# Optimization experiments

Hardware: AMD Instinct MI355X
Metric: run time of the kernel (lower is better)

Reference implementation:

```python
import jax, jax.numpy as jnp
import numpy as np
from jax import lax

CHANNEL_N = 16
ALPHA_CHANNEL = 3
FIRE_RATE = 0.5


def get_sobel(size):
    # generalized Sobel: g(x,y) = x / (x^2 + y^2), zero at center
    s = size // 2
    yy, xx = np.mgrid[-s:s + 1, -s:s + 1].astype(np.float32)
    denom = xx * xx + yy * yy
    denom[s, s] = 1.0
    gx = xx / denom
    gy = yy / denom
    gx /= np.sum(np.abs(gx))
    gy /= np.sum(np.abs(gy))
    return gx, gy


def build_kernel(C):
    # stack the six sobel stencils (sizes 3/5/7), zero-padded to 7x7 so a single
    # SAME depthwise conv reproduces the three separate padded convs exactly
    ks = []
    for size in (3, 5, 7):
        gx, gy = get_sobel(size)
        p = (7 - size) // 2
        ks.append(np.pad(gx, p))
        ks.append(np.pad(gy, p))
    k = np.stack(ks, 0)                # [6,7,7]
    k = np.tile(k, (C, 1, 1))          # [6C,7,7], channel-major groups
    return jnp.asarray(k.transpose(1, 2, 0)[:, :, None, :])  # HWIO [7,7,1,6C]


def _maxpool(x, size):
    p = size // 2
    return lax.reduce_window(x, -jnp.inf, lax.max, (1, size, size, 1), (1, 1, 1, 1),
                             [(0, 0), (p, p), (p, p), (0, 0)])


def _life_mask(x):
    alpha = x[..., ALPHA_CHANNEL:ALPHA_CHANNEL + 1]
    return _maxpool(alpha, 3) > 0.1


def _update(x, stoch_u, valid_mask, kern, W0, b0, W1):
    N, H, W, C = x.shape
    pre_life = _life_mask(x)
    y = lax.conv_general_dilated(x, kern, (1, 1), [(3, 3), (3, 3)],
                                 dimension_numbers=("NHWC", "HWIO", "NHWC"),
                                 feature_group_count=C)  # [N,H,W,6C] channel-major
    # reorder to (y1 all C, y2 all C, ...) matching torch.cat order
    y = y.reshape(N, H, W, C, 6).transpose(0, 1, 2, 4, 3).reshape(N, H, W, 6 * C)
    perc = jnp.concatenate([x, y, _maxpool(x, 5)], axis=-1)  # [N,H,W,8C]
    h = jax.nn.relu(perc @ W0 + b0)  # [N,H,W,256]
    dx = h @ W1                      # [N,H,W,C]
    dx = dx * (stoch_u > FIRE_RATE).astype(x.dtype)
    x = x + dx
    life = (pre_life & _life_mask(x)).astype(x.dtype)
    return x * life * valid_mask


def setup_inputs():
    key = jax.random.key(0)
    k1, k2, k3, k4 = jax.random.split(key, 4)
    B, H, W, C, steps = 8, 256, 256, CHANNEL_N, 16
    x = jax.random.uniform(k1, (B, H, W, C), jnp.float32)
    valid_mask = jnp.ones((B, H, W, 1), jnp.float32)
    stoch = jax.random.uniform(k2, (steps, B, H, W, 1), jnp.float32)
    W0 = jax.random.normal(k3, (8 * C, 256), jnp.float32) * 0.05
    b0 = jnp.zeros((256,), jnp.float32)
    W1 = jax.random.normal(k4, (256, C), jnp.float32) * 0.02
    return {"x": x, "valid_mask": valid_mask, "stoch": stoch,
            "W0": W0, "b0": b0, "W1": W1, "steps": steps}


def reference(x, valid_mask, stoch, W0, b0, W1, steps):
    kern = build_kernel(x.shape[-1])

    def step(carry, su):
        return _update(carry, su, valid_mask, kern, W0, b0, W1), None

    x, _ = lax.scan(step, x, stoch[:steps])
    return x
```

## Files before the change

### kernel.cpp

```cpp
#include <hip/hip_runtime.h>
#include <math.h>


#define HW 256
#define NPIX (8*HW*HW)

typedef __attribute__((ext_vector_type(8))) short short8;
typedef __attribute__((ext_vector_type(4))) float f32x4;

__device__ __forceinline__ float4 f4max(float4 a, float4 b) {
    return make_float4(fmaxf(a.x,b.x), fmaxf(a.y,b.y), fmaxf(a.z,b.z), fmaxf(a.w,b.w));
}
__device__ __forceinline__ unsigned short bf16_rne(float v) {
    unsigned int u = __float_as_uint(v);
    unsigned int r = u + 0x7FFFu + ((u >> 16) & 1u);
    return (unsigned short)(r >> 16);
}
__device__ __forceinline__ float bf16f(unsigned short h) {
    return __uint_as_float(((unsigned int)h) << 16);
}

__global__ void init_kernel(const float* __restrict__ W0,
                            float* __restrict__ filt,
                            unsigned short* __restrict__ W0hiT,
                            unsigned short* __restrict__ W0loT) {
    int t = blockIdx.x * blockDim.x + threadIdx.x;
    for (int idx = t; idx < 32768; idx += gridDim.x * blockDim.x) {
        int j = idx >> 7, k = idx & 127;
        float v = W0[k * 256 + j];
        unsigned short hi = bf16_rne(v);
        unsigned short lo = bf16_rne(v - bf16f(hi));
        W0hiT[idx] = hi;
        W0loT[idx] = lo;
    }
    if (t < 6) {
        int f = t;
        int size = 3 + 2*(f >> 1);
        int p0 = (7 - size) >> 1;
        int isY = f & 1;
        float vals[49];
        float norm = 0.f;
        for (int a = 0; a < 7; a++) {
            for (int b = 0; b < 7; b++) {
                float v = 0.f;
                if (a >= p0 && a < p0+size && b >= p0 && b < p0+size) {
                    float fy = (float)(a - 3), fx = (float)(b - 3);
                    float den = fx*fx + fy*fy;
                    if (den == 0.f) den = 1.f;
                    v = (isY ? fy : fx) / den;
                }
                vals[a*7+b] = v;
                norm += fabsf(v);
            }
        }
        float inv = 1.f / norm;
        for (int i = 0; i < 49; i++) filt[f*49 + i] = vals[i] * inv;
    }
}

__launch_bounds__(256, 2)
__global__ void step_main(const float* __restrict__ x,
                          float* __restrict__ xmid,
                          const unsigned char* __restrict__ prelife_in,
                          unsigned char* __restrict__ prelife_out,
                          const float* __restrict__ filt_g,
                          const unsigned short* __restrict__ W0hiT,
                          const unsigned short* __restrict__ W0loT,
                          const float* __restrict__ b0,
                          const float* __restrict__ W1,
                          const float* __restrict__ stoch_s,
                          const float* __restrict__ valid,
                          int apply_mask) {
    __shared__ float smem[16640];
    float*          xs      = smem;
    float*          filt_s  = smem + 3920;
    unsigned short* w0h     = (unsigned short*)smem;
    unsigned short* w0l     = (unsigned short*)(smem + 2176);
    unsigned short* perc_hi = (unsigned short*)(smem + 4352);
    unsigned short* perc_lo = (unsigned short*)(smem + 8704);
    float*          hbuf    = smem + 13056;
    float*          xcen    = smem + 15360;

    const int t   = threadIdx.x;
    const int b   = blockIdx.z;
    const int ty0 = blockIdx.y * 8;
    const int tx0 = blockIdx.x * 8;

    const int sgbase = ((t >> 3) << 7) + ((t & 7) << 4);
    const int swds   = (t >> 3) * 136 + ((t & 7) << 4);
    uint4 sh0 = *(const uint4*)&W0hiT[sgbase];
    uint4 sh1 = *(const uint4*)&W0hiT[sgbase + 8];
    uint4 sl0 = *(const uint4*)&W0loT[sgbase];
    uint4 sl1 = *(const uint4*)&W0loT[sgbase + 8];

    for (int i = t; i < 294; i += 256) filt_s[i] = filt_g[i];

    if (t < 196) {
        const int ly = t / 14, lx = t - ly*14;
        const int gy = ty0 + ly - 3, gx = tx0 + lx - 3;
        const bool inb = ((unsigned)gy < 256u) && ((unsigned)gx < 256u);
        float4 v0 = make_float4(0.f,0.f,0.f,0.f), v1 = v0, v2 = v0, v3 = v0;
        if (inb) {
            const int pix = (b << 16) + (gy << 8) + gx;
            const float* srcp = &x[(size_t)pix << 4];
            v0 = *(const float4*)(srcp);
            v1 = *(const float4*)(srcp + 4);
            v2 = *(const float4*)(srcp + 8);
            v3 = *(const float4*)(srcp + 12);
            if (apply_mask) {
                float m = -INFINITY;
                #pragma unroll
                for (int dy = -1; dy <= 1; dy++) {
                    #pragma unroll
                    for (int dxo = -1; dxo <= 1; dxo++) {
                        int yy = gy + dy, xx2 = gx + dxo;
                        if ((unsigned)yy < 256u && (unsigned)xx2 < 256u)
                            m = fmaxf(m, x[((size_t)((b<<16)+(yy<<8)+xx2) << 4) + 3]);
                    }
                }
                float s = (prelife_in[pix] != 0 && m > 0.1f) ? valid[pix] : 0.f;
                v0.x *= s; v0.y *= s; v0.z *= s; v0.w *= s;
                v1.x *= s; v1.y *= s; v1.z *= s; v1.w *= s;
                v2.x *= s; v2.y *= s; v2.z *= s; v2.w *= s;
                v3.x *= s; v3.y *= s; v3.z *= s; v3.w *= s;
            }
        }
        float* dstp = &xs[t * 20];
        *(float4*)(dstp)      = v0;
        *(float4*)(dstp + 4)  = v1;
        *(float4*)(dstp + 8)  = v2;
        *(float4*)(dstp + 12) = v3;
    }
    __syncthreads();

    {
        const int p  = t & 63;
        const int q  = t >> 6;
        const int py = p >> 3, px1 = p & 7;
        const int gy = ty0 + py, gx = tx0 + px1;
        const int q4 = q << 2;

        float4 y4[6];
        #pragma unroll
        for (int f = 0; f < 6; f++) y4[f] = make_float4(0.f,0.f,0.f,0.f);

        #pragma unroll
        for (int a = 0; a < 7; a++) {
            #pragma unroll
            for (int bb = 0; bb < 7; bb++) {
                float4 xv = *(const float4*)&xs[((py+a)*14 + (px1+bb))*20 + q4];
                {
                    float w4 = filt_s[4*49 + a*7 + bb];
                    float w5 = filt_s[5*49 + a*7 + bb];
                    y4[4].x = fmaf(w4, xv.x, y4[4].x); y4[4].y = fmaf(w4, xv.y, y4[4].y);
                    y4[4].z = fmaf(w4, xv.z, y4[4].z); y4[4].w = fmaf(w4, xv.w, y4[4].w);
                    y4[5].x = fmaf(w5, xv.x, y4[5].x); y4[5].y = fmaf(w5, xv.y, y4[5].y);
                    y4[5].z = fmaf(w5, xv.z, y4[5].z); y4[5].w = fmaf(w5, xv.w, y4[5].w);
                }
                if (a >= 1 && a <= 5 && bb >= 1 && bb <= 5) {
                    float w2 = filt_s[2*49 + a*7 + bb];
                    float w3 = filt_s[3*49 + a*7 + bb];
                    y4[2].x = fmaf(w2, xv.x, y4[2].x); y4[2].y = fmaf(w2, xv.y, y4[2].y);
                    y4[2].z = fmaf(w2, xv.z, y4[2].z); y4[2].w = fmaf(w2, xv.w, y4[2].w);
                    y4[3].x = fmaf(w3, xv.x, y4[3].x); y4[3].y = fmaf(w3, xv.y, y4[3].y);
                    y4[3].z = fmaf(w3, xv.z, y4[3].z); y4[3].w = fmaf(w3, xv.w, y4[3].w);
                }
                if (a >= 2 && a <= 4 && bb >= 2 && bb <= 4) {
                    float w0 = filt_s[0*49 + a*7 + bb];
                    float w1 = filt_s[1*49 + a*7 + bb];
                    y4[0].x = fmaf(w0, xv.x, y4[0].x); y4[0].y = fmaf(w0, xv.y, y4[0].y);
                    y4[0].z = fmaf(w0, xv.z, y4[0].z); y4[0].w = fmaf(w0, xv.w, y4[0].w);
                    y4[1].x = fmaf(w1, xv.x, y4[1].x); y4[1].y = fmaf(w1, xv.y, y4[1].y);
                    y4[1].z = fmaf(w1, xv.z, y4[1].z); y4[1].w = fmaf(w1, xv.w, y4[1].w);
                }
            }
        }
        float4 m5 = make_float4(-INFINITY,-INFINITY,-INFINITY,-INFINITY);
        #pragma unroll
        for (int dy = -2; dy <= 2; dy++) {
            #pragma unroll
            for (int dx2 = -2; dx2 <= 2; dx2++) {
                if ((unsigned)(gy+dy) < 256u && (unsigned)(gx+dx2) < 256u)
                    m5 = f4max(m5, *(const float4*)&xs[((py+3+dy)*14 + (px1+3+dx2))*20 + q4]);
            }
        }
        float4 xc = *(const float4*)&xs[((py+3)*14 + (px1+3))*20 + q4];

        #define SPLIT4(arridx, v) { \
            unsigned short h0 = bf16_rne((v).x), h1 = bf16_rne((v).y); \
            unsigned short h2 = bf16_rne((v).z), h3 = bf16_rne((v).w); \
            unsigned short l0 = bf16_rne((v).x - bf16f(h0)); \
            unsigned short l1 = bf16_rne((v).y - bf16f(h1)); \
            unsigned short l2 = bf16_rne((v).z - bf16f(h2)); \
            unsigned short l3 = bf16_rne((v).w - bf16f(h3)); \
            *(ushort4*)&perc_hi[arridx] = make_ushort4(h0,h1,h2,h3); \
            *(ushort4*)&perc_lo[arridx] = make_ushort4(l0,l1,l2,l3); }

        const int prow = p * 136;
        SPLIT4(prow +       q4, xc);
        SPLIT4(prow + 16  + q4, y4[0]);
        SPLIT4(prow + 32  + q4, y4[1]);
        SPLIT4(prow + 48  + q4, y4[2]);
        SPLIT4(prow + 64  + q4, y4[3]);
        SPLIT4(prow + 80  + q4, y4[4]);
        SPLIT4(prow + 96  + q4, y4[5]);
        SPLIT4(prow + 112 + q4, m5);
        #undef SPLIT4

        *(float4*)&xcen[p*20 + q4] = xc;

        if (q == 0) {
            float pre = -INFINITY;
            #pragma unroll
            for (int dy = -1; dy <= 1; dy++) {
                #pragma unroll
                for (int dx2 = -1; dx2 <= 1; dx2++) {
                    if ((unsigned)(gy+dy) < 256u && (unsigned)(gx+dx2) < 256u)
                        pre = fmaxf(pre, xs[((py+3+dy)*14 + (px1+3+dx2))*20 + 3]);
                }
            }
            prelife_out[(b << 16) + (gy << 8) + gx] = (pre > 0.1f) ? 1 : 0;
        }
    }
    __syncthreads();

    const int lane = t & 63;
    const int wid  = t >> 6;
    const int l15  = lane & 15;
    const int l4   = lane >> 4;
    const int aoff = (wid*16 + l15)*136 + 8*l4;
    const int boff0 = (l15)*136 + 8*l4;
    const int boff1 = (16 + l15)*136 + 8*l4;
    const int hrow  = wid*16 + 4*l4;

    const int kq   = t & 3;
    const int jg   = (t >> 2) & 3;
    const int quad = t >> 4;
    const int jg8  = jg << 3;
    const int p0px = quad << 2;

    float dx[4][4];
    #pragma unroll
    for (int i = 0; i < 4; i++)
        #pragma unroll
        for (int c = 0; c < 4; c++) dx[i][c] = 0.f;

    *(uint4*)&w0h[swds]     = sh0;
    *(uint4*)&w0h[swds + 8] = sh1;
    *(uint4*)&w0l[swds]     = sl0;
    *(uint4*)&w0l[swds + 8] = sl1;
    sh0 = *(const uint4*)&W0hiT[sgbase + 4096];
    sh1 = *(const uint4*)&W0hiT[sgbase + 4096 + 8];
    sl0 = *(const uint4*)&W0loT[sgbase + 4096];
    sl1 = *(const uint4*)&W0loT[sgbase + 4096 + 8];
    __syncthreads();

    #pragma unroll 1
    for (int jc = 0; jc < 8; jc++) {
        short8 ah0 = *(const short8*)&perc_hi[aoff +  0];
        short8 ah1 = *(const short8*)&perc_hi[aoff + 32];
        short8 ah2 = *(const short8*)&perc_hi[aoff + 64];
        short8 ah3 = *(const short8*)&perc_hi[aoff + 96];
        short8 al0 = *(const short8*)&perc_lo[aoff +  0];
        short8 al1 = *(const short8*)&perc_lo[aoff + 32];
        short8 al2 = *(const short8*)&perc_lo[aoff + 64];
        short8 al3 = *(const short8*)&perc_lo[aoff + 96];

        f32x4 acc0 = {0.f, 0.f, 0.f, 0.f};
        f32x4 acc1 = {0.f, 0.f, 0.f, 0.f};

        #define KSTEP(accv, boff, AH, AL, ks) { \
            short8 bh = *(const short8*)&w0h[(boff) + (ks)*32]; \
            short8 bl = *(const short8*)&w0l[(boff) + (ks)*32]; \
            accv = __builtin_amdgcn_mfma_f32_16x16x32_bf16(AL, bh, accv, 0, 0, 0); \
            accv = __builtin_amdgcn_mfma_f32_16x16x32_bf16(AH, bl, accv, 0, 0, 0); \
            accv = __builtin_amdgcn_mfma_f32_16x16x32_bf16(AH, bh, accv, 0, 0, 0); }

        KSTEP(acc0, boff0, ah0, al0, 0)
        KSTEP(acc0, boff0, ah1, al1, 1)
        KSTEP(acc0, boff0, ah2, al2, 2)
        KSTEP(acc0, boff0, ah3, al3, 3)
        KSTEP(acc1, boff1, ah0, al0, 0)
        KSTEP(acc1, boff1, ah1, al1, 1)
        KSTEP(acc1, boff1, ah2, al2, 2)
        KSTEP(acc1, boff1, ah3, al3, 3)
        #undef KSTEP

        {
            float bias0 = b0[jc*32 + l15];
            float bias1 = b0[jc*32 + 16 + l15];
            hbuf[(hrow+0)*36 + l15]      = fmaxf(acc0[0] + bias0, 0.f);
            hbuf[(hrow+1)*36 + l15]      = fmaxf(acc0[1] + bias0, 0.f);
            hbuf[(hrow+2)*36 + l15]      = fmaxf(acc0[2] + bias0, 0.f);
            hbuf[(hrow+3)*36 + l15]      = fmaxf(acc0[3] + bias0, 0.f);
            hbuf[(hrow+0)*36 + 16 + l15] = fmaxf(acc1[0] + bias1, 0.f);
            hbuf[(hrow+1)*36 + 16 + l15] = fmaxf(acc1[1] + bias1, 0.f);
            hbuf[(hrow+2)*36 + 16 + l15] = fmaxf(acc1[2] + bias1, 0.f);
            hbuf[(hrow+3)*36 + 16 + l15] = fmaxf(acc1[3] + bias1, 0.f);
        }
        __syncthreads();

        if (jc < 7) {
            *(uint4*)&w0h[swds]     = sh0;
            *(uint4*)&w0h[swds + 8] = sh1;
            *(uint4*)&w0l[swds]     = sl0;
            *(uint4*)&w0l[swds + 8] = sl1;
        }

        const int jbase = (jc << 5) + jg8;
        #pragma unroll
        for (int i = 0; i < 4; i++) {
            const float* hp = &hbuf[(p0px + i)*36 + jg8];
            float4 hA = *(const float4*)hp;
            float4 hB = *(const float4*)(hp + 4);
            #pragma unroll
            for (int jj = 0; jj < 8; jj++) {
                float hv = jj==0?hA.x : jj==1?hA.y : jj==2?hA.z : jj==3?hA.w :
                           jj==4?hB.x : jj==5?hB.y : jj==6?hB.z : hB.w;
                float4 wv = *(const float4*)&W1[((jbase + jj) << 4) + (kq << 2)];
                dx[i][0] = fmaf(hv, wv.x, dx[i][0]);
                dx[i][1] = fmaf(hv, wv.y, dx[i][1]);
                dx[i][2] = fmaf(hv, wv.z, dx[i][2]);
                dx[i][3] = fmaf(hv, wv.w, dx[i][3]);
            }
        }

        if (jc < 7) {
            __syncthreads();
            if (jc < 6) {
                const int nb = sgbase + (jc + 2) * 4096;
                sh0 = *(const uint4*)&W0hiT[nb];
                sh1 = *(const uint4*)&W0hiT[nb + 8];
                sl0 = *(const uint4*)&W0loT[nb];
                sl1 = *(const uint4*)&W0loT[nb + 8];
            }
        }
    }

    #pragma unroll
    for (int i = 0; i < 4; i++)
        #pragma unroll
        for (int c = 0; c < 4; c++) {
            dx[i][c] += __shfl_xor(dx[i][c], 4);
            dx[i][c] += __shfl_xor(dx[i][c], 8);
        }

    float o0 = jg==0?dx[0][0] : jg==1?dx[1][0] : jg==2?dx[2][0] : dx[3][0];
    float o1 = jg==0?dx[0][1] : jg==1?dx[1][1] : jg==2?dx[2][1] : dx[3][1];
    float o2 = jg==0?dx[0][2] : jg==1?dx[1][2] : jg==2?dx[2][2] : dx[3][2];
    float o3 = jg==0?dx[0][3] : jg==1?dx[1][3] : jg==2?dx[2][3] : dx[3][3];

    const int pw  = p0px + jg;
    const int ppy = pw >> 3, ppx = pw & 7;
    const int pix2 = (b << 16) + ((ty0 + ppy) << 8) + (tx0 + ppx);
    float fire = (stoch_s[pix2] > 0.5f) ? 1.f : 0.f;
    float4 xc2 = *(const float4*)&xcen[pw*20 + (kq << 2)];
    float4 xn;
    xn.x = fmaf(fire, o0, xc2.x);
    xn.y = fmaf(fire, o1, xc2.y);
    xn.z = fmaf(fire, o2, xc2.z);
    xn.w = fmaf(fire, o3, xc2.w);
    *(float4*)&xmid[((size_t)pix2 << 4) + (kq << 2)] = xn;
}

__global__ void step_mask(float* __restrict__ xbuf,
                          const unsigned char* __restrict__ prelife,
                          const float* __restrict__ valid) {
    int pix = blockIdx.x * 256 + threadIdx.x;
    int b = pix >> 16;
    int y = (pix >> 8) & 255;
    int x = pix & 255;
    float m = -INFINITY;
    #pragma unroll
    for (int dy = -1; dy <= 1; dy++) {
        #pragma unroll
        for (int dxo = -1; dxo <= 1; dxo++) {
            int yy = y + dy, xx = x + dxo;
            if ((unsigned)yy < 256u && (unsigned)xx < 256u)
                m = fmaxf(m, xbuf[((size_t)((b << 16) + (yy << 8) + xx) << 4) + 3]);
        }
    }
    float s = (prelife[pix] != 0 && m > 0.1f) ? valid[pix] : 0.f;
    float4* xp = (float4*)&xbuf[(size_t)pix << 4];
    #pragma unroll
    for (int i = 0; i < 4; i++) {
        float4 v = xp[i];
        v.x *= s; v.y *= s; v.z *= s; v.w *= s;
        xp[i] = v;
    }
}

extern "C" void kernel_launch(void* const* d_in, const int* in_sizes, int n_in,
                              void* d_out, int out_size, void* d_ws, size_t ws_size,
                              hipStream_t stream) {
    const float* x0    = (const float*)d_in[0];
    const float* valid = (const float*)d_in[1];
    const float* stoch = (const float*)d_in[2];
    const float* W0    = (const float*)d_in[3];
    const float* b0    = (const float*)d_in[4];
    const float* W1    = (const float*)d_in[5];

    float* ws   = (float*)d_ws;
    float* xA   = ws;
    unsigned char* plA = (unsigned char*)(ws + 8388608);
    unsigned char* plB = plA + 524288;
    float* filt = ws + 8650752;
    unsigned short* W0hiT = (unsigned short*)(ws + 8651072);
    unsigned short* W0loT = (unsigned short*)(ws + 8667456);
    float* out  = (float*)d_out;

    init_kernel<<<128, 256, 0, stream>>>(W0, filt, W0hiT, W0loT);

    const float* src = x0;
    for (int k = 1; k <= 16; k++) {
        float* dst = (k & 1) ? xA : out;
        unsigned char* wr = (k & 1) ? plB : plA;
        unsigned char* rd = (k & 1) ? plA : plB;
        step_main<<<dim3(32,32,8), 256, 0, stream>>>(
            src, dst, rd, wr, filt, W0hiT, W0loT, b0, W1,
            stoch + (size_t)(k-1)*NPIX, valid, (k > 1) ? 1 : 0);
        src = dst;
    }
    step_mask<<<NPIX/256, 256, 0, stream>>>(out, plA, valid);
}
```

Baseline: 11.23 ms.

## Move second matmul to split-bf16 MFMA and double-buffer W0 tiles in LDS

Replaces the scalar FMA loop for h @ W1 with bf16 hi/lo split MFMA instructions, using a W1 layout precomputed in the init kernel. Hidden activations are kept per-wave in LDS as bf16 hi/lo pairs. W0 chunks are double-buffered in shared memory, which removes one barrier per iteration, and the A fragments are hoisted out of the loop. The center x is rebuilt from the hi+lo perc values rather than a separate buffer. This can lose a little precision, and the larger LDS footprint may reduce occupancy.

```diff
diff --git a/kernel.cpp b/kernel.cpp
--- a/kernel.cpp
+++ b/kernel.cpp
@@ -21,17 +21,29 @@
 }
 
 __global__ void init_kernel(const float* __restrict__ W0,
+                            const float* __restrict__ W1,
                             float* __restrict__ filt,
                             unsigned short* __restrict__ W0hiT,
-                            unsigned short* __restrict__ W0loT) {
+                            unsigned short* __restrict__ W0loT,
+                            unsigned short* __restrict__ W1hiT2,
+                            unsigned short* __restrict__ W1loT2) {
     int t = blockIdx.x * blockDim.x + threadIdx.x;
-    for (int idx = t; idx < 32768; idx += gridDim.x * blockDim.x) {
+    int nth = gridDim.x * blockDim.x;
+    for (int idx = t; idx < 32768; idx += nth) {
         int j = idx >> 7, k = idx & 127;
         float v = W0[k * 256 + j];
         unsigned short hi = bf16_rne(v);
         unsigned short lo = bf16_rne(v - bf16f(hi));
         W0hiT[idx] = hi;
         W0loT[idx] = lo;
+    }
+    for (int idx = t; idx < 4096; idx += nth) {
+        int ch = idx >> 8, j = idx & 255;
+        float v = W1[j * 16 + ch];
+        unsigned short hi = bf16_rne(v);
+        unsigned short lo = bf16_rne(v - bf16f(hi));
+        W1hiT2[idx] = hi;
+        W1loT2[idx] = lo;
     }
     if (t < 6) {
         int f = t;
@@ -66,20 +78,23 @@
                           const float* __restrict__ filt_g,
                           const unsigned short* __restrict__ W0hiT,
                           const unsigned short* __restrict__ W0loT,
+                          const unsigned short* __restrict__ W1hiT2,
+                          const unsigned short* __restrict__ W1loT2,
                           const float* __restrict__ b0,
-                          const float* __restrict__ W1,
                           const float* __restrict__ stoch_s,
                           const float* __restrict__ valid,
                           int apply_mask) {
-    __shared__ float smem[16640];
+    __shared__ float smem[19712];
     float*          xs      = smem;
     float*          filt_s  = smem + 3920;
-    unsigned short* w0h     = (unsigned short*)smem;
-    unsigned short* w0l     = (unsigned short*)(smem + 2176);
-    unsigned short* perc_hi = (unsigned short*)(smem + 4352);
-    unsigned short* perc_lo = (unsigned short*)(smem + 8704);
-    float*          hbuf    = smem + 13056;
-    float*          xcen    = smem + 15360;
+    unsigned short* w0hA    = (unsigned short*)smem;
+    unsigned short* w0lA    = (unsigned short*)(smem + 2176);
+    unsigned short* w0hB    = (unsigned short*)(smem + 4352);
+    unsigned short* w0lB    = (unsigned short*)(smem + 6528);
+    unsigned short* perc_hi = (unsigned short*)(smem + 8704);
+    unsigned short* perc_lo = (unsigned short*)(smem + 13056);
+    unsigned short* hbuf_hi = (unsigned short*)(smem + 17408);
+    unsigned short* hbuf_lo = (unsigned short*)(smem + 18560);
 
     const int t   = threadIdx.x;
     const int b   = blockIdx.z;
@@ -207,8 +222,6 @@
         SPLIT4(prow + 112 + q4, m5);
         #undef SPLIT4
 
-        *(float4*)&xcen[p*20 + q4] = xc;
-
         if (q == 0) {
             float pre = -INFINITY;
             #pragma unroll
@@ -228,27 +241,28 @@
     const int wid  = t >> 6;
     const int l15  = lane & 15;
     const int l4   = lane >> 4;
-    const int aoff = (wid*16 + l15)*136 + 8*l4;
+    const int aoff  = (wid*16 + l15)*136 + 8*l4;
     const int boff0 = (l15)*136 + 8*l4;
     const int boff1 = (16 + l15)*136 + 8*l4;
-    const int hrow  = wid*16 + 4*l4;
-
-    const int kq   = t & 3;
-    const int jg   = (t >> 2) & 3;
-    const int quad = t >> 4;
-    const int jg8  = jg << 3;
-    const int p0px = quad << 2;
-
-    float dx[4][4];
-    #pragma unroll
-    for (int i = 0; i < 4; i++)
-        #pragma unroll
-        for (int c = 0; c < 4; c++) dx[i][c] = 0.f;
-
-    *(uint4*)&w0h[swds]     = sh0;
-    *(uint4*)&w0h[swds + 8] = sh1;
-    *(uint4*)&w0l[swds]     = sl0;
-    *(uint4*)&w0l[swds + 8] = sl1;
+    const int hwr   = (wid*16 + 4*l4)*36 + l15;
+    const int hrd   = (wid*16 + l15)*36 + 8*l4;
+    const int w1off = l15*256 + 8*l4;
+
+    short8 ah0 = *(const short8*)&perc_hi[aoff +  0];
+    short8 ah1 = *(const short8*)&perc_hi[aoff + 32];
+    short8 ah2 = *(const short8*)&perc_hi[aoff + 64];
+    short8 ah3 = *(const short8*)&perc_hi[aoff + 96];
+    short8 al0 = *(const short8*)&perc_lo[aoff +  0];
+    short8 al1 = *(const short8*)&perc_lo[aoff + 32];
+    short8 al2 = *(const short8*)&perc_lo[aoff + 64];
+    short8 al3 = *(const short8*)&perc_lo[aoff + 96];
+
+    f32x4 dacc = {0.f, 0.f, 0.f, 0.f};
+
+    *(uint4*)&w0hA[swds]     = sh0;
+    *(uint4*)&w0hA[swds + 8] = sh1;
+    *(uint4*)&w0lA[swds]     = sl0;
+    *(uint4*)&w0lA[swds + 8] = sl1;
     sh0 = *(const uint4*)&W0hiT[sgbase + 4096];
     sh1 = *(const uint4*)&W0hiT[sgbase + 4096 + 8];
     sl0 = *(const uint4*)&W0loT[sgbase + 4096];
@@ -257,21 +271,17 @@
 
     #pragma unroll 1
     for (int jc = 0; jc < 8; jc++) {
-        short8 ah0 = *(const short8*)&perc_hi[aoff +  0];
-        short8 ah1 = *(const short8*)&perc_hi[aoff + 32];
-        short8 ah2 = *(const short8*)&perc_hi[aoff + 64];
-        short8 ah3 = *(const short8*)&perc_hi[aoff + 96];
-        short8 al0 = *(const short8*)&perc_lo[aoff +  0];
-        short8 al1 = *(const short8*)&perc_lo[aoff + 32];
-        short8 al2 = *(const short8*)&perc_lo[aoff + 64];
-        short8 al3 = *(const short8*)&perc_lo[aoff + 96];
+        const unsigned short* wrdh = (jc & 1) ? w0hB : w0hA;
+        const unsigned short* wrdl = (jc & 1) ? w0lB : w0lA;
+        unsigned short*       wwrh = (jc & 1) ? w0hA : w0hB;
+        unsigned short*       wwrl = (jc & 1) ? w0lA : w0lB;
 
         f32x4 acc0 = {0.f, 0.f, 0.f, 0.f};
         f32x4 acc1 = {0.f, 0.f, 0.f, 0.f};
 
         #define KSTEP(accv, boff, AH, AL, ks) { \
-            short8 bh = *(const short8*)&w0h[(boff) + (ks)*32]; \
-            short8 bl = *(const short8*)&w0l[(boff) + (ks)*32]; \
+            short8 bh = *(const short8*)&wrdh[(boff) + (ks)*32]; \
+            short8 bl = *(const short8*)&wrdl[(boff) + (ks)*32]; \
             accv = __builtin_amdgcn_mfma_f32_16x16x32_bf16(AL, bh, accv, 0, 0, 0); \
             accv = __builtin_amdgcn_mfma_f32_16x16x32_bf16(AH, bl, accv, 0, 0, 0); \
             accv = __builtin_amdgcn_mfma_f32_16x16x32_bf16(AH, bh, accv, 0, 0, 0); }
@@ -289,44 +299,36 @@
         {
             float bias0 = b0[jc*32 + l15];
             float bias1 = b0[jc*32 + 16 + l15];
-            hbuf[(hrow+0)*36 + l15]      = fmaxf(acc0[0] + bias0, 0.f);
-            hbuf[(hrow+1)*36 + l15]      = fmaxf(acc0[1] + bias0, 0.f);
-            hbuf[(hrow+2)*36 + l15]      = fmaxf(acc0[2] + bias0, 0.f);
-            hbuf[(hrow+3)*36 + l15]      = fmaxf(acc0[3] + bias0, 0.f);
-            hbuf[(hrow+0)*36 + 16 + l15] = fmaxf(acc1[0] + bias1, 0.f);
-            hbuf[(hrow+1)*36 + 16 + l15] = fmaxf(acc1[1] + bias1, 0.f);
-            hbuf[(hrow+2)*36 + 16 + l15] = fmaxf(acc1[2] + bias1, 0.f);
-            hbuf[(hrow+3)*36 + 16 + l15] = fmaxf(acc1[3] + bias1, 0.f);
-        }
-        __syncthreads();
+            #pragma unroll
+            for (int r = 0; r < 4; r++) {
+                float h0 = fmaxf(acc0[r] + bias0, 0.f);
+                float h1 = fmaxf(acc1[r] + bias1, 0.f);
+                unsigned short hh0 = bf16_rne(h0);
+                unsigned short hl0 = bf16_rne(h0 - bf16f(hh0));
+                unsigned short hh1 = bf16_rne(h1);
+                unsigned short hl1 = bf16_rne(h1 - bf16f(hh1));
+                hbuf_hi[hwr + r*36]      = hh0;
+                hbuf_lo[hwr + r*36]      = hl0;
+                hbuf_hi[hwr + r*36 + 16] = hh1;
+                hbuf_lo[hwr + r*36 + 16] = hl1;
+            }
+        }
+
+        {
+            short8 hhf = *(const short8*)&hbuf_hi[hrd];
+            short8 hlf = *(const short8*)&hbuf_lo[hrd];
+            short8 w1h = *(const short8*)&W1hiT2[w1off + jc*32];
+            short8 w1l = *(const short8*)&W1loT2[w1off + jc*32];
+            dacc = __builtin_amdgcn_mfma_f32_16x16x32_bf16(hlf, w1h, dacc, 0, 0, 0);
+            dacc = __builtin_amdgcn_mfma_f32_16x16x32_bf16(hhf, w1l, dacc, 0, 0, 0);
+            dacc = __builtin_amdgcn_mfma_f32_16x16x32_bf16(hhf, w1h, dacc, 0, 0, 0);
+        }
 
         if (jc < 7) {
-            *(uint4*)&w0h[swds]     = sh0;
-            *(uint4*)&w0h[swds + 8] = sh1;
-            *(uint4*)&w0l[swds]     = sl0;
-            *(uint4*)&w0l[swds + 8] = sl1;
-        }
-
-        const int jbase = (jc << 5) + jg8;
-        #pragma unroll
-        for (int i = 0; i < 4; i++) {
-            const float* hp = &hbuf[(p0px + i)*36 + jg8];
-            float4 hA = *(const float4*)hp;
-            float4 hB = *(const float4*)(hp + 4);
-            #pragma unroll
-            for (int jj = 0; jj < 8; jj++) {
-                float hv = jj==0?hA.x : jj==1?hA.y : jj==2?hA.z : jj==3?hA.w :
-                           jj==4?hB.x : jj==5?hB.y : jj==6?hB.z : hB.w;
-                float4 wv = *(const float4*)&W1[((jbase + jj) << 4) + (kq << 2)];
-                dx[i][0] = fmaf(hv, wv.x, dx[i][0]);
-                dx[i][1] = fmaf(hv, wv.y, dx[i][1]);
-                dx[i][2] = fmaf(hv, wv.z, dx[i][2]);
-                dx[i][3] = fmaf(hv, wv.w, dx[i][3]);
-            }
-        }
-
-        if (jc < 7) {
-            __syncthreads();
+            *(uint4*)&wwrh[swds]     = sh0;
+            *(uint4*)&wwrh[swds + 8] = sh1;
+            *(uint4*)&wwrl[swds]     = sl0;
+            *(uint4*)&wwrl[swds + 8] = sl1;
             if (jc < 6) {
                 const int nb = sgbase + (jc + 2) * 4096;
                 sh0 = *(const uint4*)&W0hiT[nb];
@@ -334,33 +336,19 @@
                 sl0 = *(const uint4*)&W0loT[nb];
                 sl1 = *(const uint4*)&W0loT[nb + 8];
             }
-        }
-    }
-
+            __syncthreads();
+        }
+    }
+
+    const int pxb = wid*16 + 4*l4;
     #pragma unroll
-    for (int i = 0; i < 4; i++)
-        #pragma unroll
-        for (int c = 0; c < 4; c++) {
-            dx[i][c] += __shfl_xor(dx[i][c], 4);
-            dx[i][c] += __shfl_xor(dx[i][c], 8);
-        }
-
-    float o0 = jg==0?dx[0][0] : jg==1?dx[1][0] : jg==2?dx[2][0] : dx[3][0];
-    float o1 = jg==0?dx[0][1] : jg==1?dx[1][1] : jg==2?dx[2][1] : dx[3][1];
-    float o2 = jg==0?dx[0][2] : jg==1?dx[1][2] : jg==2?dx[2][2] : dx[3][2];
-    float o3 = jg==0?dx[0][3] : jg==1?dx[1][3] : jg==2?dx[2][3] : dx[3][3];
-
-    const int pw  = p0px + jg;
-    const int ppy = pw >> 3, ppx = pw & 7;
-    const int pix2 = (b << 16) + ((ty0 + ppy) << 8) + (tx0 + ppx);
-    float fire = (stoch_s[pix2] > 0.5f) ? 1.f : 0.f;
-    float4 xc2 = *(const float4*)&xcen[pw*20 + (kq << 2)];
-    float4 xn;
-    xn.x = fmaf(fire, o0, xc2.x);
-    xn.y = fmaf(fire, o1, xc2.y);
-    xn.z = fmaf(fire, o2, xc2.z);
-    xn.w = fmaf(fire, o3, xc2.w);
-    *(float4*)&xmid[((size_t)pix2 << 4) + (kq << 2)] = xn;
+    for (int r = 0; r < 4; r++) {
+        const int px   = pxb + r;
+        const int pix2 = (b << 16) + ((ty0 + (px >> 3)) << 8) + (tx0 + (px & 7));
+        float fire = (stoch_s[pix2] > 0.5f) ? 1.f : 0.f;
+        float xc = bf16f(perc_hi[px*136 + l15]) + bf16f(perc_lo[px*136 + l15]);
+        xmid[((size_t)pix2 << 4) + l15] = fmaf(fire, dacc[r], xc);
+    }
 }
 
 __global__ void step_mask(float* __restrict__ xbuf,
@@ -405,11 +393,14 @@
     unsigned char* plA = (unsigned char*)(ws + 8388608);
     unsigned char* plB = plA + 524288;
     float* filt = ws + 8650752;
-    unsigned short* W0hiT = (unsigned short*)(ws + 8651072);
-    unsigned short* W0loT = (unsigned short*)(ws + 8667456);
+    unsigned short* W0hiT  = (unsigned short*)(ws + 8651072);
+    unsigned short* W0loT  = (unsigned short*)(ws + 8667456);
+    unsigned short* W1hiT2 = (unsigned short*)(ws + 8683840);
+    unsigned short* W1loT2 = (unsigned short*)(ws + 8685888);
     float* out  = (float*)d_out;
 
-    init_kernel<<<128, 256, 0, stream>>>(W0, filt, W0hiT, W0loT);
+    init_kernel<<<128, 256, 0, stream>>>(W0, W1, filt, W0hiT, W0loT,
+                                         W1hiT2, W1loT2);
 
     const float* src = x0;
     for (int k = 1; k <= 16; k++) {
@@ -417,7 +408,7 @@
         unsigned char* wr = (k & 1) ? plB : plA;
         unsigned char* rd = (k & 1) ? plA : plB;
         step_main<<<dim3(32,32,8), 256, 0, stream>>>(
-            src, dst, rd, wr, filt, W0hiT, W0loT, b0, W1,
+            src, dst, rd, wr, filt, W0hiT, W0loT, W1hiT2, W1loT2, b0,
             stoch + (size_t)(k-1)*NPIX, valid, (k > 1) ? 1 : 0);
         src = dst;
     }
```

After: 10.60 ms (median of 3 runs). -5.6%, faster.
